# Optimization experiments

Hardware: AMD Instinct MI355X
Metric: run time of the kernel (lower is better)

Reference implementation:

```python
import jax, jax.numpy as jnp
import numpy as np

B, N, D = 8, 8192, 512
HID_ATT = D // 8          # input_dim // num_heads = 64
TOPK = max(1, int(N * 0.3))  # 2457


def _mlp2(x, W1, b1, W2, b2):
    # 2-layer MLP: Linear -> GELU -> Linear (inference mode: dropout/norm off)
    h = jax.nn.gelu(x @ W1 + b1)
    return h @ W2 + b2


def setup_inputs() -> dict:
    key = jax.random.key(0)
    ks = jax.random.split(key, 9)
    s = lambda k, sh, fan: jax.random.normal(k, sh, jnp.float32) * (1.0 / np.sqrt(fan))
    return {
        "x": jax.random.normal(ks[0], (B, N, D), jnp.float32),
        # attention-score MLP: D -> HID_ATT -> 1
        "aW1": s(ks[1], (D, HID_ATT), D),
        "ab1": jnp.zeros((HID_ATT,), jnp.float32),
        "aW2": s(ks[2], (HID_ATT, 1), HID_ATT),
        "ab2": jnp.zeros((1,), jnp.float32),
        # projection MLP: D -> D -> D
        "pW1": s(ks[3], (D, D), D),
        "pb1": jnp.zeros((D,), jnp.float32),
        "pW2": s(ks[4], (D, D), D),
        "pb2": jnp.zeros((D,), jnp.float32),
    }


def reference(x, aW1, ab1, aW2, ab2, pW1, pb1, pW2, pb2):
    # per-instance attention score -> sigmoid weight, [B, N]
    weights = jax.nn.sigmoid(_mlp2(x, aW1, ab1, aW2, ab2)[..., 0])
    # top-k per bag (largest)
    topk_scores, topk_idx = jax.lax.top_k(weights, TOPK)  # [B, TOPK]
    # gather selected instances, scale by score, mean over selected -> [B, D]
    sel = jnp.take_along_axis(x, topk_idx[..., None], axis=1)  # [B, TOPK, D]
    emb = jnp.mean(sel * topk_scores[..., None], axis=1)       # [B, D]
    projection = _mlp2(emb, pW1, pb1, pW2, pb2)                # [B, D]
    return projection, weights
```

## Files before the change

kernel.cpp:

```cpp
#include <hip/hip_runtime.h>
#include <math.h>

#define B_BAGS 8
#define N_INST 8192
#define D_DIM  512
#define H_ATT  64
#define TOPK_K 2457
#define ROWS_TOTAL (B_BAGS * N_INST)

typedef __attribute__((ext_vector_type(8))) short bf16x8;
typedef __attribute__((ext_vector_type(4))) float f32x4;
typedef __attribute__((ext_vector_type(4))) unsigned short u16x4;

#define WS_W1T_HI 0
#define WS_W1T_LO 65536
#define WS_META   131072
#define WS_PART3  131584
#define WS_PART1  (WS_PART3 + 8*32*512*4)
#define WS_PART2  (WS_PART1 + 8*8*512*4)

__device__ __forceinline__ unsigned short bf16_rn(float f) {
  unsigned int x = __float_as_uint(f);
  unsigned int r = (x + 0x7FFFu + ((x >> 16) & 1u)) >> 16;
  return (unsigned short)r;
}
__device__ __forceinline__ float bf16_f(unsigned short u) {
  return __uint_as_float(((unsigned int)u) << 16);
}
__device__ __forceinline__ float gelu_f(float v) {
  float u = 0.7978845608028654f * (v + 0.044715f * v * v * v);
  return 0.5f * v * (1.0f + tanhf(u));
}

__global__ __launch_bounds__(256) void k_prep(const float* __restrict__ aW1,
                                              unsigned short* __restrict__ hi,
                                              unsigned short* __restrict__ lo) {
  int o = blockIdx.x * 256 + threadIdx.x;
  if (o >= H_ATT * D_DIM) return;
  int n = o >> 9;
  int k = o & 511;
  float v = aW1[k * H_ATT + n];
  unsigned short h = bf16_rn(v);
  unsigned short l = bf16_rn(v - bf16_f(h));
  hi[o] = h;
  lo[o] = l;
}

#define BM 128
#define BK 64
#define LDK 72

__global__ __launch_bounds__(256, 2) void k_scores(
    const float* __restrict__ x,
    const unsigned short* __restrict__ w1t_hi,
    const unsigned short* __restrict__ w1t_lo,
    const float* __restrict__ ab1, const float* __restrict__ aW2,
    const float* __restrict__ ab2, float* __restrict__ wout) {
  __shared__ unsigned short A_hi[BM * LDK];
  __shared__ unsigned short A_lo[BM * LDK];
  __shared__ unsigned short Bh[H_ATT * LDK];
  __shared__ unsigned short Bl[H_ATT * LDK];

  int tid = threadIdx.x;
  int wave = tid >> 6, lane = tid & 63;
  int rowBase = blockIdx.x * BM;

  f32x4 acc[2][4];
#pragma unroll
  for (int s = 0; s < 2; s++)
#pragma unroll
    for (int t = 0; t < 4; t++) acc[s][t] = (f32x4){0.f, 0.f, 0.f, 0.f};

  for (int kc = 0; kc < D_DIM; kc += BK) {
#pragma unroll
    for (int i = 0; i < 8; i++) {
      int idx = tid + i * 256;
      int r = idx >> 4;
      int kk = (idx & 15) << 2;
      const float4 v = *reinterpret_cast<const float4*>(
          x + (size_t)(rowBase + r) * D_DIM + kc + kk);
      unsigned short h0 = bf16_rn(v.x), h1 = bf16_rn(v.y), h2 = bf16_rn(v.z), h3 = bf16_rn(v.w);
      unsigned short l0 = bf16_rn(v.x - bf16_f(h0));
      unsigned short l1 = bf16_rn(v.y - bf16_f(h1));
      unsigned short l2 = bf16_rn(v.z - bf16_f(h2));
      unsigned short l3 = bf16_rn(v.w - bf16_f(h3));
      int a = r * LDK + kk;
      *reinterpret_cast<u16x4*>(&A_hi[a]) = (u16x4){h0, h1, h2, h3};
      *reinterpret_cast<u16x4*>(&A_lo[a]) = (u16x4){l0, l1, l2, l3};
    }
#pragma unroll
    for (int i = 0; i < 2; i++) {
      int idx = tid + i * 256;
      int n = idx >> 3;
      int kk = (idx & 7) << 3;
      *reinterpret_cast<int4*>(&Bh[n * LDK + kk]) =
          *reinterpret_cast<const int4*>(w1t_hi + n * D_DIM + kc + kk);
      *reinterpret_cast<int4*>(&Bl[n * LDK + kk]) =
          *reinterpret_cast<const int4*>(w1t_lo + n * D_DIM + kc + kk);
    }
    __syncthreads();

#pragma unroll
    for (int k2 = 0; k2 < 2; k2++) {
      int ko = k2 * 32 + (lane >> 4) * 8;
      bf16x8 afh[2], afl[2], bfh[4], bfl[4];
#pragma unroll
      for (int s = 0; s < 2; s++) {
        int r = wave * 32 + s * 16 + (lane & 15);
        afh[s] = *reinterpret_cast<const bf16x8*>(&A_hi[r * LDK + ko]);
        afl[s] = *reinterpret_cast<const bf16x8*>(&A_lo[r * LDK + ko]);
      }
#pragma unroll
      for (int t = 0; t < 4; t++) {
        int n = t * 16 + (lane & 15);
        bfh[t] = *reinterpret_cast<const bf16x8*>(&Bh[n * LDK + ko]);
        bfl[t] = *reinterpret_cast<const bf16x8*>(&Bl[n * LDK + ko]);
      }
#pragma unroll
      for (int s = 0; s < 2; s++)
#pragma unroll
        for (int t = 0; t < 4; t++) {
          acc[s][t] = __builtin_amdgcn_mfma_f32_16x16x32_bf16(afl[s], bfh[t], acc[s][t], 0, 0, 0);
          acc[s][t] = __builtin_amdgcn_mfma_f32_16x16x32_bf16(afh[s], bfl[t], acc[s][t], 0, 0, 0);
          acc[s][t] = __builtin_amdgcn_mfma_f32_16x16x32_bf16(afh[s], bfh[t], acc[s][t], 0, 0, 0);
        }
    }
    __syncthreads();
  }

  int c0 = lane & 15, quad = lane >> 4;
  float w2v[4], b1v[4];
#pragma unroll
  for (int t = 0; t < 4; t++) {
    w2v[t] = aW2[t * 16 + c0];
    b1v[t] = ab1[t * 16 + c0];
  }
  float bias2 = ab2[0];
#pragma unroll
  for (int s = 0; s < 2; s++) {
    float p[4] = {0.f, 0.f, 0.f, 0.f};
#pragma unroll
    for (int t = 0; t < 4; t++)
#pragma unroll
      for (int r = 0; r < 4; r++) {
        float h = gelu_f(acc[s][t][r] + b1v[t]);
        p[r] += h * w2v[t];
      }
#pragma unroll
    for (int off = 1; off < 16; off <<= 1)
#pragma unroll
      for (int r = 0; r < 4; r++) p[r] += __shfl_xor(p[r], off, 64);
    if (c0 == 0) {
      int row = rowBase + wave * 32 + s * 16 + quad * 4;
#pragma unroll
      for (int r = 0; r < 4; r++) {
        float sc = p[r] + bias2;
        wout[row + r] = 1.0f / (1.0f + expf(-sc));
      }
    }
  }
}

__global__ __launch_bounds__(256) void k_topk(const float* __restrict__ wout,
                                              unsigned int* __restrict__ meta) {
  int b = blockIdx.x;
  const float* w = wout + b * N_INST;
  int tid = threadIdx.x;
  unsigned int v[32];
#pragma unroll
  for (int j = 0; j < 32; j++) v[j] = __float_as_uint(w[j * 256 + tid]);

  __shared__ int red[4];
  __shared__ int bc;
  int lane = tid & 63, wv = tid >> 6;

  unsigned int lo = 0u, hi = 0x3F800001u;
  while (hi - lo > 1u) {
    unsigned int mid = lo + ((hi - lo) >> 1);
    int c = 0;
#pragma unroll
    for (int j = 0; j < 32; j++) c += (v[j] >= mid) ? 1 : 0;
#pragma unroll
    for (int off = 32; off > 0; off >>= 1) c += __shfl_down(c, off, 64);
    if (lane == 0) red[wv] = c;
    __syncthreads();
    if (tid == 0) bc = red[0] + red[1] + red[2] + red[3];
    __syncthreads();
    if (bc >= TOPK_K) lo = mid; else hi = mid;
  }
  unsigned int T = lo;

  {
    int c = 0;
#pragma unroll
    for (int j = 0; j < 32; j++) c += (v[j] > T) ? 1 : 0;
#pragma unroll
    for (int off = 32; off > 0; off >>= 1) c += __shfl_down(c, off, 64);
    __syncthreads();
    if (lane == 0) red[wv] = c;
    __syncthreads();
    if (tid == 0) bc = red[0] + red[1] + red[2] + red[3];
    __syncthreads();
  }
  int needed = TOPK_K - bc;

  int lom = -1, him = N_INST - 1;
  while (him - lom > 1) {
    int mid = (lom + him) >> 1;
    int c = 0;
#pragma unroll
    for (int j = 0; j < 32; j++) c += (v[j] == T && (j * 256 + tid) <= mid) ? 1 : 0;
#pragma unroll
    for (int off = 32; off > 0; off >>= 1) c += __shfl_down(c, off, 64);
    __syncthreads();
    if (lane == 0) red[wv] = c;
    __syncthreads();
    if (tid == 0) bc = red[0] + red[1] + red[2] + red[3];
    __syncthreads();
    if (bc >= needed) him = mid; else lom = mid;
  }
  if (tid == 0) {
    meta[b] = T;
    ((int*)meta)[8 + b] = him;
  }
}

__global__ __launch_bounds__(256) void k_gather(const float* __restrict__ x,
                                                const float* __restrict__ wout,
                                                const unsigned int* __restrict__ meta,
                                                float* __restrict__ part3) {
  int b = blockIdx.x >> 5;
  int blk = blockIdx.x & 31;
  unsigned int T = meta[b];
  int Icut = ((const int*)meta)[8 + b];
  int tid = threadIdx.x;
  int r0 = blk * 256;

  __shared__ int idxs[256];
  __shared__ float wgts[256];
  __shared__ int wcnt[4];

  int r = r0 + tid;
  float wvv = wout[b * N_INST + r];
  unsigned int wu = __float_as_uint(wvv);
  bool sel = (wu > T) || (wu == T && r <= Icut);
  unsigned long long m = __ballot(sel);
  int lane = tid & 63, wave = tid >> 6;
  int pos = __popcll(m & ((1ull << lane) - 1ull));
  if (lane == 0) wcnt[wave] = __popcll(m);
  __syncthreads();
  int base = 0;
  for (int i = 0; i < wave; i++) base += wcnt[i];
  int total = wcnt[0] + wcnt[1] + wcnt[2] + wcnt[3];
  if (sel) {
    idxs[base + pos] = r;
    wgts[base + pos] = wvv;
  }
  __syncthreads();

  float2 acc = {0.f, 0.f};
  const float* xb = x + (size_t)b * N_INST * D_DIM;
#pragma unroll 4
  for (int i = 0; i < total; i++) {
    int rr = idxs[i];
    float ww = wgts[i];
    const float2 xv = *reinterpret_cast<const float2*>(xb + (size_t)rr * D_DIM + tid * 2);
    acc.x += ww * xv.x;
    acc.y += ww * xv.y;
  }
  *reinterpret_cast<float2*>(part3 + (size_t)(b * 32 + blk) * D_DIM + tid * 2) = acc;
}

__global__ __launch_bounds__(512) void k_proj1(const float* __restrict__ part3,
                                               const float* __restrict__ pW1,
                                               float* __restrict__ part1) {
  int s = blockIdx.x;
  __shared__ float emb_s[8][64];
  int tid = threadIdx.x;
  int b = tid >> 6, d = tid & 63;
  int dd = s * 64 + d;
  float e = 0.f;
#pragma unroll 8
  for (int j = 0; j < 32; j++) e += part3[(b * 32 + j) * D_DIM + dd];
  emb_s[b][d] = e * (1.0f / TOPK_K);
  __syncthreads();
  float accv[8] = {0.f, 0.f, 0.f, 0.f, 0.f, 0.f, 0.f, 0.f};
  for (int q = 0; q < 64; q++) {
    float wq = pW1[(s * 64 + q) * D_DIM + tid];
#pragma unroll
    for (int bb = 0; bb < 8; bb++) accv[bb] += emb_s[bb][q] * wq;
  }
#pragma unroll
  for (int bb = 0; bb < 8; bb++) part1[(s * 8 + bb) * D_DIM + tid] = accv[bb];
}

__global__ __launch_bounds__(512) void k_proj2(const float* __restrict__ part1,
                                               const float* __restrict__ pb1,
                                               const float* __restrict__ pW2,
                                               float* __restrict__ part2) {
  int s = blockIdx.x;
  __shared__ float h1_s[8][64];
  int tid = threadIdx.x;
  int b = tid >> 6, d = tid & 63;
  int dd = s * 64 + d;
  float hsum = pb1[dd];
#pragma unroll
  for (int j = 0; j < 8; j++) hsum += part1[(j * 8 + b) * D_DIM + dd];
  h1_s[b][d] = gelu_f(hsum);
  __syncthreads();
  float accv[8] = {0.f, 0.f, 0.f, 0.f, 0.f, 0.f, 0.f, 0.f};
  for (int q = 0; q < 64; q++) {
    float wq = pW2[(s * 64 + q) * D_DIM + tid];
#pragma unroll
    for (int bb = 0; bb < 8; bb++) accv[bb] += h1_s[bb][q] * wq;
  }
#pragma unroll
  for (int bb = 0; bb < 8; bb++) part2[(s * 8 + bb) * D_DIM + tid] = accv[bb];
}

__global__ __launch_bounds__(512) void k_proj3(const float* __restrict__ part2,
                                               const float* __restrict__ pb2,
                                               float* __restrict__ out) {
  int b = blockIdx.x;
  int tid = threadIdx.x;
  float sv = pb2[tid];
#pragma unroll
  for (int j = 0; j < 8; j++) sv += part2[(j * 8 + b) * D_DIM + tid];
  out[b * D_DIM + tid] = sv;
}

extern "C" void kernel_launch(void* const* d_in, const int* in_sizes, int n_in,
                              void* d_out, int out_size, void* d_ws, size_t ws_size,
                              hipStream_t stream) {
  (void)in_sizes; (void)n_in; (void)out_size; (void)ws_size;
  const float* x   = (const float*)d_in[0];
  const float* aW1 = (const float*)d_in[1];
  const float* ab1 = (const float*)d_in[2];
  const float* aW2 = (const float*)d_in[3];
  const float* ab2 = (const float*)d_in[4];
  const float* pW1 = (const float*)d_in[5];
  const float* pb1 = (const float*)d_in[6];
  const float* pW2 = (const float*)d_in[7];
  const float* pb2 = (const float*)d_in[8];

  float* out  = (float*)d_out;
  float* wout = out + B_BAGS * D_DIM;

  char* ws = (char*)d_ws;
  unsigned short* w1t_hi = (unsigned short*)(ws + WS_W1T_HI);
  unsigned short* w1t_lo = (unsigned short*)(ws + WS_W1T_LO);
  unsigned int*   meta   = (unsigned int*)(ws + WS_META);
  float* part3 = (float*)(ws + WS_PART3);
  float* part1 = (float*)(ws + WS_PART1);
  float* part2 = (float*)(ws + WS_PART2);

  k_prep<<<dim3((H_ATT * D_DIM + 255) / 256), dim3(256), 0, stream>>>(aW1, w1t_hi, w1t_lo);
  k_scores<<<dim3(ROWS_TOTAL / BM), dim3(256), 0, stream>>>(x, w1t_hi, w1t_lo, ab1, aW2, ab2, wout);
  k_topk<<<dim3(B_BAGS), dim3(256), 0, stream>>>(wout, meta);
  k_gather<<<dim3(B_BAGS * 32), dim3(256), 0, stream>>>(x, wout, meta, part3);
  k_proj1<<<dim3(8), dim3(512), 0, stream>>>(part3, pW1, part1);
  k_proj2<<<dim3(8), dim3(512), 0, stream>>>(part1, pb1, pW2, part2);
  k_proj3<<<dim3(B_BAGS), dim3(512), 0, stream>>>(part2, pb2, out);
}
```

Measured before the change: 281.7 us.

## Prefetch score tiles into registers, streamline top-k, widen gather and projection grids

The score GEMM now loads the next K-chunk of x and W1 into registers while the MFMAs for the current chunk run, which overlaps global load latency with compute. Top-k drops one barrier per reduction round by double-buffering the shared partials, and the tie-break search uses a precomputed bitmask with popcount instead of rescanning all values. Gather uses 64 blocks per bag of 128 rows each instead of 32 blocks of 256. Both projection GEMVs are split over 64 blocks instead of 8. The cost is more register pressure in the score kernel and more partial sums to reduce.

```diff
diff --git a/kernel.cpp b/kernel.cpp
--- a/kernel.cpp
+++ b/kernel.cpp
@@ -16,7 +16,7 @@
 #define WS_W1T_LO 65536
 #define WS_META   131072
 #define WS_PART3  131584
-#define WS_PART1  (WS_PART3 + 8*32*512*4)
+#define WS_PART1  (WS_PART3 + 8*64*512*4)
 #define WS_PART2  (WS_PART1 + 8*8*512*4)
 
 __device__ __forceinline__ unsigned short bf16_rn(float f) {
@@ -71,20 +71,36 @@
 #pragma unroll
     for (int t = 0; t < 4; t++) acc[s][t] = (f32x4){0.f, 0.f, 0.f, 0.f};
 
-  for (int kc = 0; kc < D_DIM; kc += BK) {
+  float4 xa[8];
+  int4 wbh[2], wbl[2];
+
+  auto issue = [&](int kc) {
 #pragma unroll
     for (int i = 0; i < 8; i++) {
+      int r = (tid >> 4) + i * 16;
+      int kk = (tid & 15) << 2;
+      xa[i] = *reinterpret_cast<const float4*>(
+          x + (size_t)(rowBase + r) * D_DIM + kc + kk);
+    }
+#pragma unroll
+    for (int i = 0; i < 2; i++) {
       int idx = tid + i * 256;
-      int r = idx >> 4;
-      int kk = (idx & 15) << 2;
-      const float4 v = *reinterpret_cast<const float4*>(
-          x + (size_t)(rowBase + r) * D_DIM + kc + kk);
+      int n = idx >> 3;
+      int kk = (idx & 7) << 3;
+      wbh[i] = *reinterpret_cast<const int4*>(w1t_hi + n * D_DIM + kc + kk);
+      wbl[i] = *reinterpret_cast<const int4*>(w1t_lo + n * D_DIM + kc + kk);
+    }
+  };
+  auto cvt_store = [&]() {
+#pragma unroll
+    for (int i = 0; i < 8; i++) {
+      const float4 v = xa[i];
       unsigned short h0 = bf16_rn(v.x), h1 = bf16_rn(v.y), h2 = bf16_rn(v.z), h3 = bf16_rn(v.w);
       unsigned short l0 = bf16_rn(v.x - bf16_f(h0));
       unsigned short l1 = bf16_rn(v.y - bf16_f(h1));
       unsigned short l2 = bf16_rn(v.z - bf16_f(h2));
       unsigned short l3 = bf16_rn(v.w - bf16_f(h3));
-      int a = r * LDK + kk;
+      int a = ((tid >> 4) + i * 16) * LDK + ((tid & 15) << 2);
       *reinterpret_cast<u16x4*>(&A_hi[a]) = (u16x4){h0, h1, h2, h3};
       *reinterpret_cast<u16x4*>(&A_lo[a]) = (u16x4){l0, l1, l2, l3};
     }
@@ -93,13 +109,11 @@
       int idx = tid + i * 256;
       int n = idx >> 3;
       int kk = (idx & 7) << 3;
-      *reinterpret_cast<int4*>(&Bh[n * LDK + kk]) =
-          *reinterpret_cast<const int4*>(w1t_hi + n * D_DIM + kc + kk);
-      *reinterpret_cast<int4*>(&Bl[n * LDK + kk]) =
-          *reinterpret_cast<const int4*>(w1t_lo + n * D_DIM + kc + kk);
-    }
-    __syncthreads();
-
+      *reinterpret_cast<int4*>(&Bh[n * LDK + kk]) = wbh[i];
+      *reinterpret_cast<int4*>(&Bl[n * LDK + kk]) = wbl[i];
+    }
+  };
+  auto mfma_phase = [&]() {
 #pragma unroll
     for (int k2 = 0; k2 < 2; k2++) {
       int ko = k2 * 32 + (lane >> 4) * 8;
@@ -125,7 +139,19 @@
           acc[s][t] = __builtin_amdgcn_mfma_f32_16x16x32_bf16(afh[s], bfh[t], acc[s][t], 0, 0, 0);
         }
     }
+  };
+
+  issue(0);
+  cvt_store();
+  __syncthreads();
+  for (int kc8 = 0; kc8 < 8; kc8++) {
+    if (kc8 < 7) issue((kc8 + 1) * BK);
+    mfma_phase();
     __syncthreads();
+    if (kc8 < 7) {
+      cvt_store();
+      __syncthreads();
+    }
   }
 
   int c0 = lane & 15, quad = lane >> 4;
@@ -170,9 +196,19 @@
 #pragma unroll
   for (int j = 0; j < 32; j++) v[j] = __float_as_uint(w[j * 256 + tid]);
 
-  __shared__ int red[4];
-  __shared__ int bc;
+  __shared__ int red[2][4];
   int lane = tid & 63, wv = tid >> 6;
+  int pb = 0;
+
+  auto blocksum = [&](int c) -> int {
+#pragma unroll
+    for (int off = 32; off > 0; off >>= 1) c += __shfl_down(c, off, 64);
+    if (lane == 0) red[pb][wv] = c;
+    __syncthreads();
+    int s = red[pb][0] + red[pb][1] + red[pb][2] + red[pb][3];
+    pb ^= 1;
+    return s;
+  };
 
   unsigned int lo = 0u, hi = 0x3F800001u;
   while (hi - lo > 1u) {
@@ -180,44 +216,33 @@
     int c = 0;
 #pragma unroll
     for (int j = 0; j < 32; j++) c += (v[j] >= mid) ? 1 : 0;
-#pragma unroll
-    for (int off = 32; off > 0; off >>= 1) c += __shfl_down(c, off, 64);
-    if (lane == 0) red[wv] = c;
-    __syncthreads();
-    if (tid == 0) bc = red[0] + red[1] + red[2] + red[3];
-    __syncthreads();
-    if (bc >= TOPK_K) lo = mid; else hi = mid;
+    int s = blocksum(c);
+    if (s >= TOPK_K) lo = mid; else hi = mid;
   }
   unsigned int T = lo;
 
+  int c1;
   {
     int c = 0;
 #pragma unroll
     for (int j = 0; j < 32; j++) c += (v[j] > T) ? 1 : 0;
-#pragma unroll
-    for (int off = 32; off > 0; off >>= 1) c += __shfl_down(c, off, 64);
-    __syncthreads();
-    if (lane == 0) red[wv] = c;
-    __syncthreads();
-    if (tid == 0) bc = red[0] + red[1] + red[2] + red[3];
-    __syncthreads();
-  }
-  int needed = TOPK_K - bc;
-
+    c1 = blocksum(c);
+  }
+  int needed = TOPK_K - c1;
+
+  unsigned int tm = 0;
+#pragma unroll
+  for (int j = 0; j < 32; j++) tm |= (v[j] == T ? 1u : 0u) << j;
   int lom = -1, him = N_INST - 1;
   while (him - lom > 1) {
     int mid = (lom + him) >> 1;
-    int c = 0;
-#pragma unroll
-    for (int j = 0; j < 32; j++) c += (v[j] == T && (j * 256 + tid) <= mid) ? 1 : 0;
-#pragma unroll
-    for (int off = 32; off > 0; off >>= 1) c += __shfl_down(c, off, 64);
-    __syncthreads();
-    if (lane == 0) red[wv] = c;
-    __syncthreads();
-    if (tid == 0) bc = red[0] + red[1] + red[2] + red[3];
-    __syncthreads();
-    if (bc >= needed) him = mid; else lom = mid;
+    unsigned int mask = 0u;
+    if (mid >= tid) {
+      unsigned int jmax = (unsigned int)(mid - tid) >> 8;
+      mask = (2u << jmax) - 1u;
+    }
+    int s = blocksum((int)__popc(tm & mask));
+    if (s >= needed) him = mid; else lom = mid;
   }
   if (tid == 0) {
     meta[b] = T;
@@ -229,30 +254,33 @@
                                                 const float* __restrict__ wout,
                                                 const unsigned int* __restrict__ meta,
                                                 float* __restrict__ part3) {
-  int b = blockIdx.x >> 5;
-  int blk = blockIdx.x & 31;
+  int b = blockIdx.x >> 6;
+  int blk = blockIdx.x & 63;
   unsigned int T = meta[b];
   int Icut = ((const int*)meta)[8 + b];
   int tid = threadIdx.x;
-  int r0 = blk * 256;
-
-  __shared__ int idxs[256];
-  __shared__ float wgts[256];
-  __shared__ int wcnt[4];
-
-  int r = r0 + tid;
-  float wvv = wout[b * N_INST + r];
-  unsigned int wu = __float_as_uint(wvv);
-  bool sel = (wu > T) || (wu == T && r <= Icut);
-  unsigned long long m = __ballot(sel);
-  int lane = tid & 63, wave = tid >> 6;
-  int pos = __popcll(m & ((1ull << lane) - 1ull));
-  if (lane == 0) wcnt[wave] = __popcll(m);
+
+  __shared__ int idxs[128];
+  __shared__ float wgts[128];
+  __shared__ int wcnt[2];
+
+  int r = blk * 128 + tid;
+  bool sel = false;
+  float wvv = 0.f;
+  int pos = 0;
+  if (tid < 128) {
+    wvv = wout[b * N_INST + r];
+    unsigned int wu = __float_as_uint(wvv);
+    sel = (wu > T) || (wu == T && r <= Icut);
+    unsigned long long m = __ballot(sel);
+    int lane = tid & 63;
+    pos = __popcll(m & ((1ull << lane) - 1ull));
+    if (lane == 0) wcnt[tid >> 6] = __popcll(m);
+  }
   __syncthreads();
-  int base = 0;
-  for (int i = 0; i < wave; i++) base += wcnt[i];
-  int total = wcnt[0] + wcnt[1] + wcnt[2] + wcnt[3];
+  int total = wcnt[0] + wcnt[1];
   if (sel) {
+    int base = (tid >= 64) ? wcnt[0] : 0;
     idxs[base + pos] = r;
     wgts[base + pos] = wvv;
   }
@@ -260,7 +288,7 @@
 
   float2 acc = {0.f, 0.f};
   const float* xb = x + (size_t)b * N_INST * D_DIM;
-#pragma unroll 4
+#pragma unroll 8
   for (int i = 0; i < total; i++) {
     int rr = idxs[i];
     float ww = wgts[i];
@@ -268,65 +296,79 @@
     acc.x += ww * xv.x;
     acc.y += ww * xv.y;
   }
-  *reinterpret_cast<float2*>(part3 + (size_t)(b * 32 + blk) * D_DIM + tid * 2) = acc;
-}
-
-__global__ __launch_bounds__(512) void k_proj1(const float* __restrict__ part3,
+  *reinterpret_cast<float2*>(part3 + (size_t)(b * 64 + blk) * D_DIM + tid * 2) = acc;
+}
+
+__global__ __launch_bounds__(256) void k_proj1(const float* __restrict__ part3,
                                                const float* __restrict__ pW1,
                                                float* __restrict__ part1) {
-  int s = blockIdx.x;
-  __shared__ float emb_s[8][64];
+  int jt = blockIdx.x & 7, kt = blockIdx.x >> 3;
+  __shared__ float emb_s[512];
   int tid = threadIdx.x;
-  int b = tid >> 6, d = tid & 63;
-  int dd = s * 64 + d;
-  float e = 0.f;
+#pragma unroll
+  for (int h = 0; h < 2; h++) {
+    int vi = tid + h * 256;
+    int b = vi >> 6, d0 = vi & 63;
+    const float* p = part3 + (size_t)b * 64 * 512 + kt * 64 + d0;
+    float e = 0.f;
 #pragma unroll 8
-  for (int j = 0; j < 32; j++) e += part3[(b * 32 + j) * D_DIM + dd];
-  emb_s[b][d] = e * (1.0f / TOPK_K);
+    for (int j = 0; j < 64; j++) e += p[j * 512];
+    emb_s[vi] = e * (1.0f / TOPK_K);
+  }
   __syncthreads();
-  float accv[8] = {0.f, 0.f, 0.f, 0.f, 0.f, 0.f, 0.f, 0.f};
+  int col = tid & 63, bg = tid >> 6;
+  float a0 = 0.f, a1 = 0.f;
+  const float* wrow = pW1 + (size_t)(kt * 64) * 512 + jt * 64 + col;
+#pragma unroll 8
   for (int q = 0; q < 64; q++) {
-    float wq = pW1[(s * 64 + q) * D_DIM + tid];
-#pragma unroll
-    for (int bb = 0; bb < 8; bb++) accv[bb] += emb_s[bb][q] * wq;
-  }
-#pragma unroll
-  for (int bb = 0; bb < 8; bb++) part1[(s * 8 + bb) * D_DIM + tid] = accv[bb];
-}
-
-__global__ __launch_bounds__(512) void k_proj2(const float* __restrict__ part1,
+    float wq = wrow[q * 512];
+    a0 += emb_s[(bg * 2) * 64 + q] * wq;
+    a1 += emb_s[(bg * 2 + 1) * 64 + q] * wq;
+  }
+  part1[kt * 4096 + (bg * 2) * 512 + jt * 64 + col] = a0;
+  part1[kt * 4096 + (bg * 2 + 1) * 512 + jt * 64 + col] = a1;
+}
+
+__global__ __launch_bounds__(256) void k_proj2(const float* __restrict__ part1,
                                                const float* __restrict__ pb1,
                                                const float* __restrict__ pW2,
                                                float* __restrict__ part2) {
-  int s = blockIdx.x;
-  __shared__ float h1_s[8][64];
+  int jt = blockIdx.x & 7, kt = blockIdx.x >> 3;
+  __shared__ float h_s[512];
   int tid = threadIdx.x;
-  int b = tid >> 6, d = tid & 63;
-  int dd = s * 64 + d;
-  float hsum = pb1[dd];
-#pragma unroll
-  for (int j = 0; j < 8; j++) hsum += part1[(j * 8 + b) * D_DIM + dd];
-  h1_s[b][d] = gelu_f(hsum);
+#pragma unroll
+  for (int h = 0; h < 2; h++) {
+    int vi = tid + h * 256;
+    int b = vi >> 6, j0 = vi & 63;
+    int jj = kt * 64 + j0;
+    float s = pb1[jj];
+#pragma unroll
+    for (int p = 0; p < 8; p++) s += part1[p * 4096 + b * 512 + jj];
+    h_s[vi] = gelu_f(s);
+  }
   __syncthreads();
-  float accv[8] = {0.f, 0.f, 0.f, 0.f, 0.f, 0.f, 0.f, 0.f};
+  int col = tid & 63, bg = tid >> 6;
+  float a0 = 0.f, a1 = 0.f;
+  const float* wrow = pW2 + (size_t)(kt * 64) * 512 + jt * 64 + col;
+#pragma unroll 8
   for (int q = 0; q < 64; q++) {
-    float wq = pW2[(s * 64 + q) * D_DIM + tid];
-#pragma unroll
-    for (int bb = 0; bb < 8; bb++) accv[bb] += h1_s[bb][q] * wq;
-  }
-#pragma unroll
-  for (int bb = 0; bb < 8; bb++) part2[(s * 8 + bb) * D_DIM + tid] = accv[bb];
+    float wq = wrow[q * 512];
+    a0 += h_s[(bg * 2) * 64 + q] * wq;
+    a1 += h_s[(bg * 2 + 1) * 64 + q] * wq;
+  }
+  part2[kt * 4096 + (bg * 2) * 512 + jt * 64 + col] = a0;
+  part2[kt * 4096 + (bg * 2 + 1) * 512 + jt * 64 + col] = a1;
 }
 
 __global__ __launch_bounds__(512) void k_proj3(const float* __restrict__ part2,
                                                const float* __restrict__ pb2,
                                                float* __restrict__ out) {
-  int b = blockIdx.x;
-  int tid = threadIdx.x;
-  float sv = pb2[tid];
-#pragma unroll
-  for (int j = 0; j < 8; j++) sv += part2[(j * 8 + b) * D_DIM + tid];
-  out[b * D_DIM + tid] = sv;
+  int o = blockIdx.x * 512 + threadIdx.x;
+  int bj = o & 511;
+  float s = pb2[bj];
+#pragma unroll
+  for (int p = 0; p < 8; p++) s += part2[p * 4096 + o];
+  out[o] = s;
 }
 
 extern "C" void kernel_launch(void* const* d_in, const int* in_sizes, int n_in,
@@ -357,8 +399,8 @@
   k_prep<<<dim3((H_ATT * D_DIM + 255) / 256), dim3(256), 0, stream>>>(aW1, w1t_hi, w1t_lo);
   k_scores<<<dim3(ROWS_TOTAL / BM), dim3(256), 0, stream>>>(x, w1t_hi, w1t_lo, ab1, aW2, ab2, wout);
   k_topk<<<dim3(B_BAGS), dim3(256), 0, stream>>>(wout, meta);
-  k_gather<<<dim3(B_BAGS * 32), dim3(256), 0, stream>>>(x, wout, meta, part3);
-  k_proj1<<<dim3(8), dim3(512), 0, stream>>>(part3, pW1, part1);
-  k_proj2<<<dim3(8), dim3(512), 0, stream>>>(part1, pb1, pW2, part2);
+  k_gather<<<dim3(B_BAGS * 64), dim3(256), 0, stream>>>(x, wout, meta, part3);
+  k_proj1<<<dim3(64), dim3(256), 0, stream>>>(part3, pW1, part1);
+  k_proj2<<<dim3(64), dim3(256), 0, stream>>>(part1, pb1, pW2, part2);
   k_proj3<<<dim3(B_BAGS), dim3(512), 0, stream>>>(part2, pb2, out);
 }
```

Result: faster. 266.5 us (-5.4%).
